# Optimization experiments

Hardware: AMD Instinct MI355X
Metric: run time of the kernel (lower is better)

## Reference

```python
import jax, jax.numpy as jnp
import numpy as np

NUM_NODES = 100000
NUM_EDGES = 50000
NUM_CONN = 800000
IN_DIM = 256
HIDDEN = 128
EDGE_ATTR_DIM = 17
LN_EPS = 1e-5


def setup_inputs() -> dict:
    key = jax.random.key(0)
    k1, k2, k3, kw1, kb1, kg, kbeta, kw2, kb2 = jax.random.split(key, 9)
    node_features = jax.random.normal(k1, (NUM_NODES, IN_DIM), dtype=jnp.float32)
    nodes = jax.random.randint(k2, (NUM_CONN,), 0, NUM_NODES, dtype=jnp.int64)
    edges = jax.random.randint(k3, (NUM_CONN,), 0, NUM_EDGES, dtype=jnp.int64)
    hyperedge_index = jnp.stack([nodes, edges], axis=0)
    # MLP params (Linear(in,hid) -> LayerNorm -> ReLU -> Dropout(eval:identity) -> Linear(hid,out))
    W1 = jax.random.normal(kw1, (IN_DIM, HIDDEN), dtype=jnp.float32) * (1.0 / np.sqrt(IN_DIM))
    b1 = jax.random.normal(kb1, (HIDDEN,), dtype=jnp.float32) * 0.01
    ln_g = jnp.ones((HIDDEN,), dtype=jnp.float32)
    ln_b = jnp.zeros((HIDDEN,), dtype=jnp.float32)
    W2 = jax.random.normal(kw2, (HIDDEN, EDGE_ATTR_DIM), dtype=jnp.float32) * (1.0 / np.sqrt(HIDDEN))
    b2 = jax.random.normal(kb2, (EDGE_ATTR_DIM,), dtype=jnp.float32) * 0.01
    return {"node_features": node_features, "hyperedge_index": hyperedge_index,
            "W1": W1, "b1": b1, "ln_g": ln_g, "ln_b": ln_b, "W2": W2, "b2": b2}


def reference(node_features, hyperedge_index, W1, b1, ln_g, ln_b, W2, b2):
    nodes = hyperedge_index[0]
    edges = hyperedge_index[1]
    # indices are in-range by construction (torch valid_mask is all-True here)
    gathered = node_features[nodes]                         # [num_conn, in_dim]
    summed = jax.ops.segment_sum(gathered, edges, num_segments=NUM_EDGES)
    counts = jax.ops.segment_sum(jnp.ones(edges.shape, node_features.dtype), edges,
                                 num_segments=NUM_EDGES)
    edge_features = summed / jnp.clip(counts, 1.0)[:, None]  # mean aggregation
    # decoder MLP (dropout inactive in eval)
    h = edge_features @ W1 + b1
    mu = jnp.mean(h, axis=-1, keepdims=True)
    var = jnp.mean(jnp.square(h - mu), axis=-1, keepdims=True)
    h = (h - mu) * jax.lax.rsqrt(var + LN_EPS) * ln_g + ln_b
    h = jax.nn.relu(h)
    return h @ W2 + b2                                      # [num_edges, edge_attr_dim]
```

## Files before the change

### kernel.cpp

```cpp
#include <hip/hip_runtime.h>
#include <hip/hip_bf16.h>
#include <stdint.h>

#define NUM_NODES 100000
#define NUM_EDGES 50000
#define NUM_CONN  800000
#define IN_DIM    256
#define HIDDEN    128
#define EDGE_DIM  17
#define PAD       64

typedef __bf16 bf16x8 __attribute__((ext_vector_type(8)));
typedef float  f32x4  __attribute__((ext_vector_type(4)));


__global__ void prep_kernel(const float* __restrict__ W1, const float* __restrict__ W2,
                            __bf16* __restrict__ w1f, __bf16* __restrict__ w2f,
                            int* __restrict__ counts) {
    int i = blockIdx.x * 256 + threadIdx.x;
    if (i < NUM_EDGES) counts[i] = 0;
    if (i < 4096) {
        int lane = i & 63, t = (i >> 6) & 7, kc2 = i >> 9;
        int m = lane & 15, q = lane >> 4;
        int n = t * 16 + m;
        int kbase = kc2 * 32 + q * 8;
        __bf16* dst = w1f + (size_t)i * 8;
        #pragma unroll
        for (int ki = 0; ki < 8; ++ki)
            dst[ki] = (__bf16)W1[(size_t)(kbase + ki) * HIDDEN + n];
    } else if (i < 4608) {
        int f = i - 4096;
        int lane = f & 63, t = (f >> 6) & 1, ks = f >> 7;
        int m = lane & 15, q = lane >> 4;
        int n = t * 16 + m;
        int kbase = ks * 32 + q * 8;
        __bf16* dst = w2f + (size_t)f * 8;
        #pragma unroll
        for (int ki = 0; ki < 8; ++ki)
            dst[ki] = (n < EDGE_DIM) ? (__bf16)W2[(size_t)(kbase + ki) * EDGE_DIM + n]
                                     : (__bf16)0.0f;
    }
}

#define FRONT_BLOCKS 3519
__global__ __launch_bounds__(256, 4) void front_kernel(const int* __restrict__ idx,
        int stride, int* __restrict__ counts, int* __restrict__ slots,
        const float* __restrict__ nf, const __bf16* __restrict__ w1f,
        __bf16* __restrict__ pbf) {
    __shared__ __align__(16) __bf16 lds_w[16384];
    if (blockIdx.x % 9 == 4) {
        int b = blockIdx.x / 9;
        long c0 = ((long)b * 256 + threadIdx.x) * 8;
        if (c0 < NUM_CONN) {
            int nd[8], ed[8];
            if (stride == 2) {
                #pragma unroll
                for (int k = 0; k < 4; ++k) {
                    int4 vn = ((const int4*)idx)[c0 / 2 + k];
                    int4 ve = ((const int4*)(idx + 2 * NUM_CONN))[c0 / 2 + k];
                    nd[2 * k] = vn.x; nd[2 * k + 1] = vn.z;
                    ed[2 * k] = ve.x; ed[2 * k + 1] = ve.z;
                }
            } else {
                #pragma unroll
                for (int k = 0; k < 8; ++k) {
                    nd[k] = idx[c0 + k];
                    ed[k] = idx[NUM_CONN + c0 + k];
                }
            }
            int pos[8];
            #pragma unroll
            for (int k = 0; k < 8; ++k) pos[k] = atomicAdd(&counts[ed[k]], 1);
            #pragma unroll
            for (int k = 0; k < 8; ++k)
                if (pos[k] < PAD) slots[(size_t)ed[k] * PAD + pos[k]] = nd[k];
        }
        return;
    }
    const int p = blockIdx.x - blockIdx.x / 9 - (blockIdx.x % 9 > 4 ? 1 : 0);
    const int rt = p >> 1;
    const int ch = p & 1;
    {
        const uint4* src = (const uint4*)w1f;
        uint4* dst = (uint4*)lds_w;
        #pragma unroll
        for (int i = threadIdx.x; i < 2048; i += 256) {
            int kc2 = i >> 8, tt = (i >> 6) & 3, lane = i & 63;
            dst[i] = src[(kc2 * 8 + ch * 4 + tt) * 64 + lane];
        }
    }
    __syncthreads();

    const int wave = threadIdx.x >> 6;
    const int lane = threadIdx.x & 63;
    const int m = lane & 15, q = lane >> 4;
    const int rowbase = rt * 256 + wave * 64;
    const bf16x8* frag = (const bf16x8*)lds_w;

    f32x4 acc[4][4];
    #pragma unroll
    for (int mt = 0; mt < 4; ++mt)
        #pragma unroll
        for (int tt = 0; tt < 4; ++tt) acc[mt][tt] = (f32x4){0.f, 0.f, 0.f, 0.f};

    const float* ap[4];
    #pragma unroll
    for (int mt = 0; mt < 4; ++mt) {
        int r = rowbase + mt * 16 + m;
        if (r >= NUM_NODES) r = NUM_NODES - 1;
        ap[mt] = nf + (size_t)r * IN_DIM + q * 8;
    }

    #pragma unroll
    for (int kc2 = 0; kc2 < 8; ++kc2) {
        bf16x8 b[4];
        #pragma unroll
        for (int tt = 0; tt < 4; ++tt) b[tt] = frag[(kc2 * 4 + tt) * 64 + lane];
        #pragma unroll
        for (int mt = 0; mt < 4; ++mt) {
            float4 f0 = *(const float4*)(ap[mt] + kc2 * 32);
            float4 f1 = *(const float4*)(ap[mt] + kc2 * 32 + 4);
            bf16x8 a;
            a[0] = (__bf16)f0.x; a[1] = (__bf16)f0.y;
            a[2] = (__bf16)f0.z; a[3] = (__bf16)f0.w;
            a[4] = (__bf16)f1.x; a[5] = (__bf16)f1.y;
            a[6] = (__bf16)f1.z; a[7] = (__bf16)f1.w;
            #pragma unroll
            for (int tt = 0; tt < 4; ++tt)
                acc[mt][tt] = __builtin_amdgcn_mfma_f32_16x16x32_bf16(a, b[tt], acc[mt][tt], 0, 0, 0);
        }
    }

    #pragma unroll
    for (int mt = 0; mt < 4; ++mt) {
        int ob = rowbase + mt * 16 + q * 4;
        #pragma unroll
        for (int tt = 0; tt < 4; ++tt) {
            int col = (ch * 4 + tt) * 16 + m;
            #pragma unroll
            for (int r = 0; r < 4; ++r) {
                int orow = ob + r;
                if (orow < NUM_NODES)
                    pbf[(size_t)orow * HIDDEN + col] = (__bf16)acc[mt][tt][r];
            }
        }
    }
}

__global__ __launch_bounds__(256) void edge_kernel(const uint4* __restrict__ p4,
        const int* __restrict__ counts, const int* __restrict__ slots,
        const float* __restrict__ b1, const float* __restrict__ ln_g,
        const float* __restrict__ ln_b, const __bf16* __restrict__ w2f,
        const float* __restrict__ b2, float* __restrict__ out) {
    __shared__ __align__(16) uint4 lds_r[256];
    const int wave = threadIdx.x >> 6;
    const int lane = threadIdx.x & 63;
    const int g = lane & 15, ge = lane >> 4;
    const int el = wave * 4 + ge;
    const int e = blockIdx.x * 16 + el;

    const int c = counts[e];
    const int cc = c < PAD ? c : PAD;
    const float inv = 1.0f / (float)(c > 0 ? c : 1);

    float acc[8];
    #pragma unroll
    for (int d = 0; d < 8; ++d) acc[d] = 0.f;

    for (int c0 = 0; c0 < cc; c0 += 16) {
        int slv = slots[(size_t)e * PAD + c0 + g];
        int lim = cc - c0; if (lim > 16) lim = 16;
        if (lim == 16) {
            #pragma unroll
            for (int k0 = 0; k0 < 16; k0 += 4) {
                uint4 u[4];
                #pragma unroll
                for (int k = 0; k < 4; ++k) {
                    int nd = __shfl(slv, ge * 16 + k0 + k, 64);
                    u[k] = p4[(size_t)nd * 16 + g];
                }
                #pragma unroll
                for (int k = 0; k < 4; ++k) {
                    acc[0] += __uint_as_float(u[k].x << 16);
                    acc[1] += __uint_as_float(u[k].x & 0xffff0000u);
                    acc[2] += __uint_as_float(u[k].y << 16);
                    acc[3] += __uint_as_float(u[k].y & 0xffff0000u);
                    acc[4] += __uint_as_float(u[k].z << 16);
                    acc[5] += __uint_as_float(u[k].z & 0xffff0000u);
                    acc[6] += __uint_as_float(u[k].w << 16);
                    acc[7] += __uint_as_float(u[k].w & 0xffff0000u);
                }
            }
        } else {
            for (int k0 = 0; k0 < lim; k0 += 4) {
                uint4 u[4];
                unsigned okm[4];
                #pragma unroll
                for (int k = 0; k < 4; ++k) {
                    int nd = __shfl(slv, ge * 16 + k0 + k, 64);
                    nd = ((unsigned)nd < NUM_NODES) ? nd : 0;
                    u[k] = p4[(size_t)nd * 16 + g];
                    okm[k] = (k0 + k < lim) ? 0xffffffffu : 0u;
                }
                #pragma unroll
                for (int k = 0; k < 4; ++k) {
                    uint4 v = u[k];
                    v.x &= okm[k]; v.y &= okm[k]; v.z &= okm[k]; v.w &= okm[k];
                    acc[0] += __uint_as_float(v.x << 16);
                    acc[1] += __uint_as_float(v.x & 0xffff0000u);
                    acc[2] += __uint_as_float(v.y << 16);
                    acc[3] += __uint_as_float(v.y & 0xffff0000u);
                    acc[4] += __uint_as_float(v.z << 16);
                    acc[5] += __uint_as_float(v.z & 0xffff0000u);
                    acc[6] += __uint_as_float(v.w << 16);
                    acc[7] += __uint_as_float(v.w & 0xffff0000u);
                }
            }
        }
    }

    float4 bA = ((const float4*)b1)[2 * g];
    float4 bB = ((const float4*)b1)[2 * g + 1];
    float h[8];
    h[0] = acc[0] * inv + bA.x; h[1] = acc[1] * inv + bA.y;
    h[2] = acc[2] * inv + bA.z; h[3] = acc[3] * inv + bA.w;
    h[4] = acc[4] * inv + bB.x; h[5] = acc[5] * inv + bB.y;
    h[6] = acc[6] * inv + bB.z; h[7] = acc[7] * inv + bB.w;

    float s = 0.f;
    #pragma unroll
    for (int d = 0; d < 8; ++d) s += h[d];
    #pragma unroll
    for (int off = 8; off > 0; off >>= 1) s += __shfl_xor(s, off, 64);
    float mu = s * (1.0f / 128.0f);

    float dv[8], vv = 0.f;
    #pragma unroll
    for (int d = 0; d < 8; ++d) { dv[d] = h[d] - mu; vv += dv[d] * dv[d]; }
    #pragma unroll
    for (int off = 8; off > 0; off >>= 1) vv += __shfl_xor(vv, off, 64);
    float rs = rsqrtf(vv * (1.0f / 128.0f) + 1e-5f);

    float4 gA = ((const float4*)ln_g)[2 * g];
    float4 gB = ((const float4*)ln_g)[2 * g + 1];
    float4 eA = ((const float4*)ln_b)[2 * g];
    float4 eB = ((const float4*)ln_b)[2 * g + 1];
    float gg[8] = {gA.x, gA.y, gA.z, gA.w, gB.x, gB.y, gB.z, gB.w};
    float ee[8] = {eA.x, eA.y, eA.z, eA.w, eB.x, eB.y, eB.z, eB.w};
    union { __bf16 b[8]; uint4 u; } pk;
    #pragma unroll
    for (int d = 0; d < 8; ++d) {
        float r = dv[d] * rs * gg[d] + ee[d];
        pk.b[d] = (__bf16)(r > 0.f ? r : 0.f);
    }
    lds_r[el * 16 + g] = pk.u;
    __syncthreads();

    if (wave == 0) {
        const int m = lane & 15, q = lane >> 4;
        const __bf16* lr = (const __bf16*)lds_r;
        const bf16x8* fw = (const bf16x8*)w2f;
        f32x4 a0 = (f32x4){0.f, 0.f, 0.f, 0.f};
        f32x4 a1 = (f32x4){0.f, 0.f, 0.f, 0.f};
        #pragma unroll
        for (int ks = 0; ks < 4; ++ks) {
            bf16x8 a = *(const bf16x8*)(lr + m * 128 + ks * 32 + q * 8);
            a0 = __builtin_amdgcn_mfma_f32_16x16x32_bf16(a, fw[(ks * 2 + 0) * 64 + lane], a0, 0, 0, 0);
            a1 = __builtin_amdgcn_mfma_f32_16x16x32_bf16(a, fw[(ks * 2 + 1) * 64 + lane], a1, 0, 0, 0);
        }
        int rowb = blockIdx.x * 16 + q * 4;
        float bm = b2[m];
        float b16 = b2[16];
        #pragma unroll
        for (int r = 0; r < 4; ++r) {
            out[(size_t)(rowb + r) * EDGE_DIM + m] = a0[r] + bm;
            if (m == 0) out[(size_t)(rowb + r) * EDGE_DIM + 16] = a1[r] + b16;
        }
    }
}

extern "C" void kernel_launch(void* const* d_in, const int* in_sizes, int n_in,
                              void* d_out, int out_size, void* d_ws, size_t ws_size,
                              hipStream_t stream) {
    const float* nf  = (const float*)d_in[0];
    const int*   idx = (const int*)d_in[1];
    const float* W1  = (const float*)d_in[2];
    const float* b1  = (const float*)d_in[3];
    const float* g   = (const float*)d_in[4];
    const float* be  = (const float*)d_in[5];
    const float* W2  = (const float*)d_in[6];
    const float* b2  = (const float*)d_in[7];
    float* out = (float*)d_out;

    char* ws = (char*)d_ws;
    __bf16* P      = (__bf16*)ws;
    int*    counts = (int*)(ws + 25600000);
    int*    slots  = (int*)(ws + 25800000);
    __bf16* W1F    = (__bf16*)(ws + 38600000);
    __bf16* W2F    = (__bf16*)(ws + 38665536);

    int stride = (in_sizes[1] == 2 * NUM_CONN) ? 1 : 2;

    prep_kernel<<<196, 256, 0, stream>>>(W1, W2, W1F, W2F, counts);
    front_kernel<<<FRONT_BLOCKS, 256, 0, stream>>>(idx, stride, counts, slots, nf, W1F, P);
    edge_kernel<<<NUM_EDGES / 16, 256, 0, stream>>>((const uint4*)P, counts, slots,
                                                    b1, g, be, W2F, b2, out);
}
```

Before: 261.4 us.

## Compute full hidden width per block and prefetch node rows into registers

The front projection kernel used to split the 128 hidden columns across two blocks, so each node row was read from global memory twice. Now each block loads the whole W1 fragment set into 64KB of LDS and computes all 128 columns for 128 rows, with each wave handling 32 rows. The second row tile's loads are issued into registers while the first tile runs its MFMAs. The scatter-block interleave changes from 1-in-9 to 1-in-3 blocks. The costs are double the LDS per block, a looser launch bound, and higher register use, which may lower occupancy.

```diff
diff --git a/kernel.cpp b/kernel.cpp
--- a/kernel.cpp
+++ b/kernel.cpp
@@ -42,15 +42,15 @@
     }
 }
 
-#define FRONT_BLOCKS 3519
-__global__ __launch_bounds__(256, 4) void front_kernel(const int* __restrict__ idx,
+#define FRONT_BLOCKS 1173
+__global__ __launch_bounds__(256) void front_kernel(const int* __restrict__ idx,
         int stride, int* __restrict__ counts, int* __restrict__ slots,
         const float* __restrict__ nf, const __bf16* __restrict__ w1f,
         __bf16* __restrict__ pbf) {
-    __shared__ __align__(16) __bf16 lds_w[16384];
-    if (blockIdx.x % 9 == 4) {
-        int b = blockIdx.x / 9;
-        long c0 = ((long)b * 256 + threadIdx.x) * 8;
+    __shared__ __align__(16) __bf16 lds_w[32768];
+    const int d3 = blockIdx.x / 3, r3 = blockIdx.x % 3;
+    if (r3 == 1) {
+        long c0 = ((long)d3 * 256 + threadIdx.x) * 8;
         if (c0 < NUM_CONN) {
             int nd[8], ed[8];
             if (stride == 2) {
@@ -77,73 +77,80 @@
         }
         return;
     }
-    const int p = blockIdx.x - blockIdx.x / 9 - (blockIdx.x % 9 > 4 ? 1 : 0);
-    const int rt = p >> 1;
-    const int ch = p & 1;
+    const int p = 2 * d3 + (r3 == 2 ? 1 : 0);
     {
         const uint4* src = (const uint4*)w1f;
         uint4* dst = (uint4*)lds_w;
         #pragma unroll
-        for (int i = threadIdx.x; i < 2048; i += 256) {
-            int kc2 = i >> 8, tt = (i >> 6) & 3, lane = i & 63;
-            dst[i] = src[(kc2 * 8 + ch * 4 + tt) * 64 + lane];
-        }
+        for (int i = threadIdx.x; i < 4096; i += 256) dst[i] = src[i];
     }
     __syncthreads();
 
     const int wave = threadIdx.x >> 6;
     const int lane = threadIdx.x & 63;
     const int m = lane & 15, q = lane >> 4;
-    const int rowbase = rt * 256 + wave * 64;
+    const int rowbase = p * 128 + wave * 32;
     const bf16x8* frag = (const bf16x8*)lds_w;
 
-    f32x4 acc[4][4];
-    #pragma unroll
-    for (int mt = 0; mt < 4; ++mt)
-        #pragma unroll
-        for (int tt = 0; tt < 4; ++tt) acc[mt][tt] = (f32x4){0.f, 0.f, 0.f, 0.f};
-
-    const float* ap[4];
-    #pragma unroll
-    for (int mt = 0; mt < 4; ++mt) {
+    const float* ap[2];
+    #pragma unroll
+    for (int mt = 0; mt < 2; ++mt) {
         int r = rowbase + mt * 16 + m;
         if (r >= NUM_NODES) r = NUM_NODES - 1;
         ap[mt] = nf + (size_t)r * IN_DIM + q * 8;
     }
 
+    f32x4 acc[2][8];
+    #pragma unroll
+    for (int mt = 0; mt < 2; ++mt)
+        #pragma unroll
+        for (int t = 0; t < 8; ++t) acc[mt][t] = (f32x4){0.f, 0.f, 0.f, 0.f};
+
+    float4 a4[16];
     #pragma unroll
     for (int kc2 = 0; kc2 < 8; ++kc2) {
-        bf16x8 b[4];
-        #pragma unroll
-        for (int tt = 0; tt < 4; ++tt) b[tt] = frag[(kc2 * 4 + tt) * 64 + lane];
-        #pragma unroll
-        for (int mt = 0; mt < 4; ++mt) {
-            float4 f0 = *(const float4*)(ap[mt] + kc2 * 32);
-            float4 f1 = *(const float4*)(ap[mt] + kc2 * 32 + 4);
-            bf16x8 a;
-            a[0] = (__bf16)f0.x; a[1] = (__bf16)f0.y;
-            a[2] = (__bf16)f0.z; a[3] = (__bf16)f0.w;
-            a[4] = (__bf16)f1.x; a[5] = (__bf16)f1.y;
-            a[6] = (__bf16)f1.z; a[7] = (__bf16)f1.w;
-            #pragma unroll
-            for (int tt = 0; tt < 4; ++tt)
-                acc[mt][tt] = __builtin_amdgcn_mfma_f32_16x16x32_bf16(a, b[tt], acc[mt][tt], 0, 0, 0);
-        }
-    }
-
-    #pragma unroll
-    for (int mt = 0; mt < 4; ++mt) {
+        a4[2 * kc2]     = *(const float4*)(ap[0] + kc2 * 32);
+        a4[2 * kc2 + 1] = *(const float4*)(ap[0] + kc2 * 32 + 4);
+    }
+
+    #pragma unroll
+    for (int mt = 0; mt < 2; ++mt) {
+        bf16x8 afr[8];
+        #pragma unroll
+        for (int kc2 = 0; kc2 < 8; ++kc2) {
+            float4 f0 = a4[2 * kc2], f1 = a4[2 * kc2 + 1];
+            afr[kc2][0] = (__bf16)f0.x; afr[kc2][1] = (__bf16)f0.y;
+            afr[kc2][2] = (__bf16)f0.z; afr[kc2][3] = (__bf16)f0.w;
+            afr[kc2][4] = (__bf16)f1.x; afr[kc2][5] = (__bf16)f1.y;
+            afr[kc2][6] = (__bf16)f1.z; afr[kc2][7] = (__bf16)f1.w;
+        }
+        if (mt == 0) {
+            #pragma unroll
+            for (int kc2 = 0; kc2 < 8; ++kc2) {
+                a4[2 * kc2]     = *(const float4*)(ap[1] + kc2 * 32);
+                a4[2 * kc2 + 1] = *(const float4*)(ap[1] + kc2 * 32 + 4);
+            }
+        }
+        #pragma unroll
+        for (int kc2 = 0; kc2 < 8; ++kc2) {
+            #pragma unroll
+            for (int t = 0; t < 8; ++t)
+                acc[mt][t] = __builtin_amdgcn_mfma_f32_16x16x32_bf16(
+                    afr[kc2], frag[(kc2 * 8 + t) * 64 + lane], acc[mt][t], 0, 0, 0);
+        }
+    }
+
+    #pragma unroll
+    for (int mt = 0; mt < 2; ++mt) {
         int ob = rowbase + mt * 16 + q * 4;
         #pragma unroll
-        for (int tt = 0; tt < 4; ++tt) {
-            int col = (ch * 4 + tt) * 16 + m;
+        for (int t = 0; t < 8; ++t)
             #pragma unroll
             for (int r = 0; r < 4; ++r) {
                 int orow = ob + r;
                 if (orow < NUM_NODES)
-                    pbf[(size_t)orow * HIDDEN + col] = (__bf16)acc[mt][tt][r];
-            }
-        }
+                    pbf[(size_t)orow * HIDDEN + t * 16 + m] = (__bf16)acc[mt][t][r];
+            }
     }
 }
 
```

After: 257.8 us. About the same (-1.4%).
